# Performance work log

Hardware: AMD Instinct MI355X
Metric: run time of the kernel (lower is better)

The kernel has to match this reference:

```python
import jax, jax.numpy as jnp
import numpy as np

B, T, C = 2, 2048, 2048
N_HEAD, N_KV = 16, 4
HD = C // N_HEAD          # 128
ROPE_THETA = 10000.0


def setup_inputs() -> dict:
    key = jax.random.key(0)
    ks = jax.random.split(key, 6)
    std = 0.02
    x = jax.random.normal(ks[0], (B, T, C), dtype=jnp.float32)
    Wq = jax.random.normal(ks[1], (C, C), dtype=jnp.float32) * std
    Wk = jax.random.normal(ks[2], (C, N_KV * HD), dtype=jnp.float32) * std
    Wv = jax.random.normal(ks[3], (C, N_KV * HD), dtype=jnp.float32) * std
    Wo = jax.random.normal(ks[4], (C, C), dtype=jnp.float32) * std
    # real RoPE frequencies: freqs_cis = exp(i * t * theta^{-2j/hd})
    inv_freq = 1.0 / (ROPE_THETA ** (jnp.arange(0, HD, 2, dtype=jnp.float32) / HD))
    ang = jnp.arange(T, dtype=jnp.float32)[:, None] * inv_freq[None, :]  # [T, HD//2]
    return {"x": x, "Wq": Wq, "Wk": Wk, "Wv": Wv, "Wo": Wo,
            "freqs_cos": jnp.cos(ang), "freqs_sin": jnp.sin(ang)}


def _rope(t, cos, sin):
    # t: [B, H, T, HD]; cos/sin: [T, HD//2] -> complex rotate even/odd pairs
    tr = t.reshape(*t.shape[:-1], HD // 2, 2)
    re, im = tr[..., 0], tr[..., 1]
    c = cos[None, None, :, :]
    s = sin[None, None, :, :]
    out = jnp.stack([re * c - im * s, re * s + im * c], axis=-1)
    return out.reshape(t.shape)


def reference(x, Wq, Wk, Wv, Wo, freqs_cos, freqs_sin):
    Bm, Tm, Cm = x.shape
    q = (x @ Wq).reshape(Bm, Tm, N_HEAD, HD).transpose(0, 2, 1, 3)  # [B,H,T,HD]
    k = (x @ Wk).reshape(Bm, Tm, N_KV, HD).transpose(0, 2, 1, 3)    # [B,Hkv,T,HD]
    v = (x @ Wv).reshape(Bm, Tm, N_KV, HD).transpose(0, 2, 1, 3)
    q = _rope(q, freqs_cos, freqs_sin)
    k = _rope(k, freqs_cos, freqs_sin)
    rep = N_HEAD // N_KV
    k = jnp.repeat(k, rep, axis=1)  # GQA repeat_kv -> [B,H,T,HD]
    v = jnp.repeat(v, rep, axis=1)
    scale = 1.0 / jnp.sqrt(jnp.asarray(HD, dtype=x.dtype))
    att = jnp.einsum("bhqd,bhkd->bhqk", q, k) * scale
    causal = jnp.tril(jnp.ones((Tm, Tm), dtype=bool))
    att = jnp.where(causal[None, None], att, jnp.asarray(-jnp.inf, att.dtype))
    att = jax.nn.softmax(att, axis=-1)
    y = jnp.einsum("bhqk,bhkd->bhqd", att, v)
    y = y.transpose(0, 2, 1, 3).reshape(Bm, Tm, Cm)
    return y @ Wo
```

## Files before the change

### kernel.cpp

```cpp
#include <hip/hip_runtime.h>

#define B_ 2
#define T_ 2048
#define C_ 2048
#define NH_ 16
#define NKV_ 4
#define HD_ 128
#define REP_ (NH_ / NKV_)
#define LDQKV 3072

typedef unsigned short u16;
typedef __bf16 bf16x8v __attribute__((ext_vector_type(8)));
typedef float f32x4v __attribute__((ext_vector_type(4)));

__device__ __forceinline__ u16 f2bf(float f) {
    unsigned int u;
    __builtin_memcpy(&u, &f, 4);
    u += 0x7FFFu + ((u >> 16) & 1u);
    return (u16)(u >> 16);
}
__device__ __forceinline__ unsigned int pk2(float a, float b) {
    unsigned int ua, ub;
    __builtin_memcpy(&ua, &a, 4);
    __builtin_memcpy(&ub, &b, 4);
    ua += 0x8000u; ub += 0x8000u;
    return (ua >> 16) | (ub & 0xFFFF0000u);
}
__device__ __forceinline__ bf16x8v load8(const u16* p) {
    return *reinterpret_cast<const bf16x8v*>(p);
}
__device__ __forceinline__ void gl16(const u16* g, u16* l) {
    __builtin_amdgcn_global_load_lds(
        (const __attribute__((address_space(1))) void*)(g),
        (__attribute__((address_space(3))) void*)(l), 16, 0, 0);
}
__device__ __forceinline__ void stg(const u16* g, u16* l, int tid, int K) {
    gl16(g, l + tid * 8);
    gl16(g + (size_t)64 * K, l + 4096 + tid * 8);
}
__device__ __forceinline__ void stgB3(const u16* g, u16* l, int tid, int K) {
    gl16(g, l + tid * 8);
    gl16(g + (size_t)64 * K, l + 4096 + tid * 8);
    gl16(g + (size_t)128 * K, l + 8192 + tid * 8);
}
#define BAR()      __builtin_amdgcn_s_barrier()
#define LGKM0()    asm volatile("s_waitcnt lgkmcnt(0)" ::: "memory")
#define SCHED0()   __builtin_amdgcn_sched_barrier(0)
#define PRIO(x)    __builtin_amdgcn_s_setprio(x)

__global__ void cvt_f32_bf16(const float* __restrict__ in, u16* __restrict__ out, int n4) {
    int i = blockIdx.x * blockDim.x + threadIdx.x;
    if (i >= n4) return;
    float4 v = reinterpret_cast<const float4*>(in)[i];
    ushort4 o;
    o.x = f2bf(v.x); o.y = f2bf(v.y); o.z = f2bf(v.z); o.w = f2bf(v.w);
    reinterpret_cast<ushort4*>(out)[i] = o;
}

__global__ void xpose_f32_bf16(const float* __restrict__ in, u16* __restrict__ out,
                               int R, int Cc) {
    __shared__ u16 tile[32][33];
    int bx = blockIdx.x * 32, by = blockIdx.y * 32;
    int tx = threadIdx.x, ty = threadIdx.y;
    for (int i = 0; i < 32; i += 8)
        tile[ty + i][tx] = f2bf(in[(size_t)(by + ty + i) * Cc + bx + tx]);
    __syncthreads();
    for (int i = 0; i < 32; i += 8)
        out[(size_t)(bx + ty + i) * R + by + tx] = tile[tx][ty + i];
}

__global__ __launch_bounds__(512, 2) void gemm_qkv(const u16* __restrict__ A,
                                                   const u16* __restrict__ BT,
                                                   u16* __restrict__ Cq,
                                                   u16* __restrict__ vtb,
                                                   const float* __restrict__ cb,
                                                   const float* __restrict__ sb,
                                                   int M, int N, int K) {
    __shared__ __align__(16) u16 As[2][2][8192];
    __shared__ __align__(16) u16 Bs[2][12288];
    int tid = threadIdx.x;
    int lane = tid & 63, wave = tid >> 6;
    int wm = wave >> 2, wn = wave & 3;
    int m15 = lane & 15, quad = lane >> 4;

    int nbx = N / 192;
    int bid = blockIdx.x, cpx = gridDim.x >> 3;
    int swz = (bid & 7) * cpx + (bid >> 3);
    int m0 = (swz / nbx) * 256, n0 = (swz % nbx) * 192;

    int r_ = tid >> 3, c_ = tid & 7;
    const u16* gA0 = A + (size_t)(m0 + r_) * K + ((c_ ^ (r_ & 7)) * 8);
    const u16* gB0 = BT + (size_t)(n0 + r_) * K + ((c_ ^ (r_ & 7)) * 8);

    int sw8 = m15 & 7;
    int co0 = (quad ^ sw8) * 8;
    int co1 = ((4 + quad) ^ sw8) * 8;
    const u16* aB = &As[0][0][0] + wm * 8192 + m15 * 64;
    const u16* bB = &Bs[0][0] + (wn * 48 + m15) * 64;

    f32x4v acc[8][3] = {};
    int NT = K >> 6;

    stgB3(gB0, &Bs[0][0], tid, K);
    stg(gA0, &As[0][0][0], tid, K);
    stg(gA0 + (size_t)128 * K, &As[0][1][0], tid, K);
    stgB3(gB0 + 64, &Bs[1][0], tid, K);
    asm volatile("s_waitcnt vmcnt(3)" ::: "memory");
    SCHED0();
    BAR();

    for (int t = 0; t < NT; t++) {
        int d = t & 1;
        const u16* aT = aB + d * 16384;
        const u16* bT = bB + d * 12288;
        bf16x8v a0[4][2], a1[4][2], bv[3][2];

#pragma unroll
        for (int mt = 0; mt < 4; mt++) {
            a0[mt][0] = load8(aT + mt * 1024 + co0);
            a0[mt][1] = load8(aT + mt * 1024 + co1);
        }
#pragma unroll
        for (int nt = 0; nt < 2; nt++) {
            bv[nt][0] = load8(bT + nt * 1024 + co0);
            bv[nt][1] = load8(bT + nt * 1024 + co1);
        }
        if (t + 1 < NT) stg(gA0 + (t + 1) * 64, &As[1 - d][0][0], tid, K);
        BAR(); LGKM0(); SCHED0(); PRIO(1);
#pragma unroll
        for (int kc = 0; kc < 2; kc++)
#pragma unroll
            for (int mt = 0; mt < 4; mt++)
#pragma unroll
                for (int nt = 0; nt < 2; nt++)
                    acc[mt][nt] = __builtin_amdgcn_mfma_f32_16x16x32_bf16(
                        a0[mt][kc], bv[nt][kc], acc[mt][nt], 0, 0, 0);
        PRIO(0); BAR();

#pragma unroll
        for (int mt = 0; mt < 4; mt++) {
            a1[mt][0] = load8(aT + (mt + 4) * 1024 + co0);
            a1[mt][1] = load8(aT + (mt + 4) * 1024 + co1);
        }
        bv[2][0] = load8(bT + 2048 + co0);
        bv[2][1] = load8(bT + 2048 + co1);
        if (t + 1 < NT) stg(gA0 + (size_t)128 * K + (t + 1) * 64, &As[1 - d][1][0], tid, K);
        BAR(); LGKM0(); SCHED0(); PRIO(1);
#pragma unroll
        for (int kc = 0; kc < 2; kc++)
#pragma unroll
            for (int mt = 0; mt < 4; mt++)
#pragma unroll
                for (int nt = 0; nt < 2; nt++)
                    acc[mt + 4][nt] = __builtin_amdgcn_mfma_f32_16x16x32_bf16(
                        a1[mt][kc], bv[nt][kc], acc[mt + 4][nt], 0, 0, 0);
        PRIO(0); BAR();

        if (t + 2 < NT) stgB3(gB0 + (t + 2) * 64, &Bs[d][0], tid, K);
        PRIO(1);
#pragma unroll
        for (int kc = 0; kc < 2; kc++)
#pragma unroll
            for (int mt = 0; mt < 4; mt++)
                acc[mt][2] = __builtin_amdgcn_mfma_f32_16x16x32_bf16(
                    a0[mt][kc], bv[2][kc], acc[mt][2], 0, 0, 0);
#pragma unroll
        for (int kc = 0; kc < 2; kc++)
#pragma unroll
            for (int mt = 0; mt < 4; mt++)
                acc[mt + 4][2] = __builtin_amdgcn_mfma_f32_16x16x32_bf16(
                    a1[mt][kc], bv[2][kc], acc[mt + 4][2], 0, 0, 0);
        PRIO(0);
        if (t + 2 < NT) { asm volatile("s_waitcnt vmcnt(3)" ::: "memory"); }
        else            { asm volatile("s_waitcnt vmcnt(0)" ::: "memory"); }
        SCHED0();
        BAR();
    }

#pragma unroll
    for (int mt = 0; mt < 8; mt++)
#pragma unroll
        for (int nt = 0; nt < 3; nt++) {
            int c = n0 + wn * 48 + nt * 16 + m15;
            if (c >= 2560) {
                int hd = c - 2560;
                int mbase = m0 + wm * 128 + mt * 16 + quad * 4;
                int bb = mbase >> 11, tok = mbase & 2047;
                int g = (tok & 31) >> 2;
                int off = (tok & ~31) + ((g & 3) * 8 + (g >> 2) * 4);
                ushort4 pk;
                pk.x = f2bf(acc[mt][nt][0]);
                pk.y = f2bf(acc[mt][nt][1]);
                pk.z = f2bf(acc[mt][nt][2]);
                pk.w = f2bf(acc[mt][nt][3]);
                *reinterpret_cast<ushort4*>(vtb + ((size_t)bb * 512 + hd) * T_ + off) = pk;
            } else {
                int i = (c & 127) >> 1;
                float sgn = (c & 1) ? 1.f : -1.f;
#pragma unroll
                for (int r = 0; r < 4; r++) {
                    int mrow = m0 + wm * 128 + mt * 16 + quad * 4 + r;
                    int tok = mrow & 2047;
                    float cv = cb[tok * 64 + i];
                    float sv = sb[tok * 64 + i];
                    float v = acc[mt][nt][r];
                    float pval = __shfl_xor(v, 1, 64);
                    float outv = fmaf(v, cv, pval * sv * sgn);
                    Cq[(size_t)mrow * N + c] = f2bf(outv);
                }
            }
        }
}

__global__ __launch_bounds__(512, 2) void gemm_out(const u16* __restrict__ A,
                                                   const u16* __restrict__ BT,
                                                   float* __restrict__ C,
                                                   int M, int N, int K) {
    __shared__ __align__(16) u16 As2[2][8192];
    __shared__ __align__(16) u16 Bs2[2][2][8192];
    int tid = threadIdx.x;
    int lane = tid & 63, wave = tid >> 6;
    int wm = wave >> 2, wn = wave & 3;
    int m15 = lane & 15, quad = lane >> 4;

    int nbx = N >> 8;
    int bid = blockIdx.x, cpx = gridDim.x >> 3;
    int swz = (bid & 7) * cpx + (bid >> 3);
    int m0 = (swz / nbx) * 128, n0 = (swz % nbx) * 256;

    const u16* gA0 = A + (size_t)(m0 + (tid >> 3)) * K + (((tid & 7) ^ ((tid >> 3) & 7)) * 8);
    const u16* gB0 = BT + (size_t)(n0 + (tid >> 3)) * K + (((tid & 7) ^ ((tid >> 3) & 7)) * 8);

    int sw8 = m15 & 7;
    int co0 = (quad ^ sw8) * 8;
    int co1 = ((4 + quad) ^ sw8) * 8;
    const u16* aB = &As2[0][0] + (wm * 64 + m15) * 64;
    const u16* bB = &Bs2[0][0][0] + (wn >> 1) * 8192 + ((wn & 1) * 64 + m15) * 64;

    f32x4v acc[4][4] = {};
    int NT = K >> 6;

    stg(gB0, &Bs2[0][0][0], tid, K);
    stg(gB0 + (size_t)128 * K, &Bs2[0][1][0], tid, K);
    stg(gA0, &As2[0][0], tid, K);
    stg(gB0 + 64, &Bs2[1][0][0], tid, K);
    stg(gB0 + (size_t)128 * K + 64, &Bs2[1][1][0], tid, K);
    asm volatile("s_waitcnt vmcnt(4)" ::: "memory");
    SCHED0();
    BAR();

    for (int t = 0; t < NT; t++) {
        int d = t & 1;
        const u16* aT = aB + d * 8192;
        const u16* bT = bB + d * 16384;
        bf16x8v a0[2][2], a1[2][2], b0[2][2], b1[2][2];

#pragma unroll
        for (int mt = 0; mt < 2; mt++) {
            a0[mt][0] = load8(aT + mt * 1024 + co0);
            a0[mt][1] = load8(aT + mt * 1024 + co1);
        }
#pragma unroll
        for (int nt = 0; nt < 2; nt++) {
            b0[nt][0] = load8(bT + nt * 1024 + co0);
            b0[nt][1] = load8(bT + nt * 1024 + co1);
        }
        if (t + 1 < NT) stg(gA0 + (t + 1) * 64, &As2[1 - d][0], tid, K);
        BAR(); LGKM0(); SCHED0(); PRIO(1);
#pragma unroll
        for (int kc = 0; kc < 2; kc++)
#pragma unroll
            for (int mt = 0; mt < 2; mt++)
#pragma unroll
                for (int nt = 0; nt < 2; nt++)
                    acc[mt][nt] = __builtin_amdgcn_mfma_f32_16x16x32_bf16(
                        a0[mt][kc], b0[nt][kc], acc[mt][nt], 0, 0, 0);
        PRIO(0); BAR();

#pragma unroll
        for (int nt = 0; nt < 2; nt++) {
            b1[nt][0] = load8(bT + (nt + 2) * 1024 + co0);
            b1[nt][1] = load8(bT + (nt + 2) * 1024 + co1);
        }
        BAR(); LGKM0(); SCHED0(); PRIO(1);
#pragma unroll
        for (int kc = 0; kc < 2; kc++)
#pragma unroll
            for (int mt = 0; mt < 2; mt++)
#pragma unroll
                for (int nt = 0; nt < 2; nt++)
                    acc[mt][nt + 2] = __builtin_amdgcn_mfma_f32_16x16x32_bf16(
                        a0[mt][kc], b1[nt][kc], acc[mt][nt + 2], 0, 0, 0);
        PRIO(0); BAR();

#pragma unroll
        for (int mt = 0; mt < 2; mt++) {
            a1[mt][0] = load8(aT + (mt + 2) * 1024 + co0);
            a1[mt][1] = load8(aT + (mt + 2) * 1024 + co1);
        }
        if (t + 2 < NT) stg(gB0 + (t + 2) * 64, &Bs2[d][0][0], tid, K);
        BAR(); LGKM0(); SCHED0(); PRIO(1);
#pragma unroll
        for (int kc = 0; kc < 2; kc++)
#pragma unroll
            for (int mt = 0; mt < 2; mt++)
#pragma unroll
                for (int nt = 0; nt < 2; nt++)
                    acc[mt + 2][nt] = __builtin_amdgcn_mfma_f32_16x16x32_bf16(
                        a1[mt][kc], b0[nt][kc], acc[mt + 2][nt], 0, 0, 0);
        PRIO(0); BAR();

        if (t + 2 < NT) stg(gB0 + (size_t)128 * K + (t + 2) * 64, &Bs2[d][1][0], tid, K);
        BAR(); PRIO(1);
#pragma unroll
        for (int kc = 0; kc < 2; kc++)
#pragma unroll
            for (int mt = 0; mt < 2; mt++)
#pragma unroll
                for (int nt = 0; nt < 2; nt++)
                    acc[mt + 2][nt + 2] = __builtin_amdgcn_mfma_f32_16x16x32_bf16(
                        a1[mt][kc], b1[nt][kc], acc[mt + 2][nt + 2], 0, 0, 0);
        PRIO(0);
        if (t + 2 < NT) { asm volatile("s_waitcnt vmcnt(4)" ::: "memory"); }
        else            { asm volatile("s_waitcnt vmcnt(0)" ::: "memory"); }
        SCHED0();
        BAR();
    }

#pragma unroll
    for (int mt = 0; mt < 4; mt++)
#pragma unroll
        for (int nt = 0; nt < 4; nt++) {
            int c = n0 + wn * 64 + nt * 16 + m15;
#pragma unroll
            for (int r = 0; r < 4; r++) {
                int mrow = m0 + wm * 64 + mt * 16 + quad * 4 + r;
                C[(size_t)mrow * N + c] = acc[mt][nt][r];
            }
        }
}

__device__ __forceinline__ void stgK64(const u16* kB, u16* Kl, int kt, int tid) {
    int keyc = tid >> 4, ch = tid & 15;
    const u16* g = kB + (size_t)(kt + keyc) * LDQKV + (ch ^ keyc) * 8;
    u16* l = Kl + tid * 8;
#pragma unroll
    for (int j = 0; j < 4; j++) {
        gl16(g, l);
        g += (size_t)16 * LDQKV;
        l += 2048;
    }
}
__device__ __forceinline__ void stgV64(const u16* vB, u16* Vl, int kt, int tid) {
    int hdc = tid >> 3, ch = tid & 7;
    const u16* g = vB + (size_t)hdc * T_ + kt + (ch ^ (hdc & 7)) * 8;
    u16* l = Vl + tid * 8;
#pragma unroll
    for (int j = 0; j < 4; j++) {
        gl16(g, l);
        g += (size_t)32 * T_;
        l += 2048;
    }
}

__global__ __launch_bounds__(256) void flash_k(const u16* __restrict__ qkv,
                                               const u16* __restrict__ vtb,
                                               u16* __restrict__ yb) {
    __shared__ __align__(16) u16 Kl[2][64 * 128];
    __shared__ __align__(16) u16 Vl[2][128 * 64];
    int h = blockIdx.y, b = blockIdx.z;
    int kv = h / REP_;
    int tid = threadIdx.x;
    int lane = tid & 63, wave = tid >> 6;
    int m15 = lane & 15, quad = lane >> 4;
    int sw8 = m15 & 7;
    const u16* kB = qkv + (size_t)b * T_ * LDQKV + 2048 + kv * HD_;
    const u16* vB = vtb + ((size_t)(b * NKV_ + kv)) * HD_ * T_;
    const float scale2 = 0.1275173723f;
    const float M0b = 8.0f;
    const float NEG = -3.0e38f;

    for (int p = 0; p < 2; p++) {
        int qt = (p == 0) ? (int)blockIdx.x : (31 - (int)blockIdx.x);
        int qt0 = qt * 64;
        int q_i = qt0 + wave * 16 + m15;
        const u16* qp = qkv + (size_t)(b * T_ + q_i) * LDQKV + h * HD_ + quad * 8;
        bf16x8v qf[4];
#pragma unroll
        for (int kc = 0; kc < 4; kc++) qf[kc] = load8(qp + kc * 32);
        f32x4v o[8] = {};
        f32x4v lacc = {};
        int NT = qt + 1;

        stgK64(kB, &Kl[0][0], 0, tid);
        stgV64(vB, &Vl[0][0], 0, tid);
        stgK64(kB, &Kl[1][0], 64, tid);
        stgV64(vB, &Vl[1][0], 64, tid);
        asm volatile("s_waitcnt vmcnt(8)" ::: "memory");
        SCHED0();
        BAR();

        for (int it = 0; it < NT; it++) {
            int cur = it & 1;
            int kt = it * 64;
            const u16* Kc = &Kl[cur][0];
            const u16* Vc = &Vl[cur][0];

            bf16x8v kf[4][4];
#pragma unroll
            for (int nt = 0; nt < 4; nt++) {
                const u16* kls = Kc + (nt * 16 + m15) * 128;
#pragma unroll
                for (int kc = 0; kc < 4; kc++)
                    kf[nt][kc] = load8(kls + (((kc * 4 + quad) ^ m15) * 8));
            }
            if (it >= 1 && it + 1 < NT) stgK64(kB, &Kl[1 - cur][0], kt + 64, tid);
            BAR(); LGKM0(); SCHED0(); PRIO(1);
            f32x4v s4[4] = {};
#pragma unroll
            for (int nt = 0; nt < 4; nt++)
#pragma unroll
                for (int kc = 0; kc < 4; kc++)
                    s4[nt] = __builtin_amdgcn_mfma_f32_16x16x32_bf16(
                        kf[nt][kc], qf[kc], s4[nt], 0, 0, 0);
            PRIO(0);
            if (it + 1 < NT) { asm volatile("s_waitcnt vmcnt(4)" ::: "memory"); }
            else             { asm volatile("s_waitcnt vmcnt(0)" ::: "memory"); }
            SCHED0(); BAR();

            if (kt + 64 > qt0) {
#pragma unroll
                for (int nt = 0; nt < 4; nt++) {
                    int key = kt + nt * 16 + quad * 4;
#pragma unroll
                    for (int r = 0; r < 4; r++)
                        if (key + r > q_i) s4[nt][r] = NEG;
                }
            }
#pragma unroll
            for (int nt = 0; nt < 4; nt++) {
#pragma unroll
                for (int r = 0; r < 4; r++)
                    s4[nt][r] = exp2f(fmaf(s4[nt][r], scale2, -M0b));
                lacc += s4[nt];
            }
            bf16x8v pf[2];
#pragma unroll
            for (int c = 0; c < 2; c++) {
                unsigned int w[4];
                w[0] = pk2(s4[2 * c][0], s4[2 * c][1]);
                w[1] = pk2(s4[2 * c][2], s4[2 * c][3]);
                w[2] = pk2(s4[2 * c + 1][0], s4[2 * c + 1][1]);
                w[3] = pk2(s4[2 * c + 1][2], s4[2 * c + 1][3]);
                __builtin_memcpy(&pf[c], w, 16);
            }
            bf16x8v vf[2][8];
#pragma unroll
            for (int c = 0; c < 2; c++)
#pragma unroll
                for (int dt = 0; dt < 8; dt++)
                    vf[c][dt] = load8(Vc + (dt * 16 + m15) * 64 + (((c * 4 + quad) ^ sw8) * 8));
            if (it >= 1 && it + 1 < NT) stgV64(vB, &Vl[1 - cur][0], kt + 64, tid);
            BAR(); LGKM0(); SCHED0(); PRIO(1);
#pragma unroll
            for (int c = 0; c < 2; c++)
#pragma unroll
                for (int dt = 0; dt < 8; dt++)
                    o[dt] = __builtin_amdgcn_mfma_f32_16x16x32_bf16(
                        vf[c][dt], pf[c], o[dt], 0, 0, 0);
            PRIO(0);
            if (it + 1 < NT) { asm volatile("s_waitcnt vmcnt(4)" ::: "memory"); }
            SCHED0(); BAR();
        }

        float l = lacc[0] + lacc[1] + lacc[2] + lacc[3];
        l += __shfl_xor(l, 16, 64);
        l += __shfl_xor(l, 32, 64);
        float inv = 1.f / l;
        u16* yp = yb + (size_t)(b * T_ + q_i) * C_ + h * HD_ + quad * 4;
#pragma unroll
        for (int dt = 0; dt < 8; dt++) {
            ushort4 pk;
            pk.x = f2bf(o[dt][0] * inv);
            pk.y = f2bf(o[dt][1] * inv);
            pk.z = f2bf(o[dt][2] * inv);
            pk.w = f2bf(o[dt][3] * inv);
            *reinterpret_cast<ushort4*>(yp + dt * 16) = pk;
        }
    }
}

extern "C" void kernel_launch(void* const* d_in, const int* in_sizes, int n_in,
                              void* d_out, int out_size, void* d_ws, size_t ws_size,
                              hipStream_t stream) {
    const float* x  = (const float*)d_in[0];
    const float* Wq = (const float*)d_in[1];
    const float* Wk = (const float*)d_in[2];
    const float* Wv = (const float*)d_in[3];
    const float* Wo = (const float*)d_in[4];
    const float* fc = (const float*)d_in[5];
    const float* fs = (const float*)d_in[6];
    float* out = (float*)d_out;

    char* ws = (char*)d_ws;
    u16* WqkvT = (u16*)(ws);
    u16* WoT   = (u16*)(ws + 12582912);
    u16* xb    = (u16*)(ws + 20971520);
    u16* qkvb  = (u16*)(ws + 37748736);
    u16* vtb   = (u16*)(ws + 62914560);
    u16* yb    = (u16*)(ws + 67108864);

    const int M = B_ * T_;

    int n4 = (M * C_) / 4;
    cvt_f32_bf16<<<n4 / 256, 256, 0, stream>>>(x, xb, n4);

    dim3 tb(32, 8);
    xpose_f32_bf16<<<dim3(C_ / 32, C_ / 32), tb, 0, stream>>>(Wq, WqkvT, C_, C_);
    xpose_f32_bf16<<<dim3((NKV_ * HD_) / 32, C_ / 32), tb, 0, stream>>>(Wk, WqkvT + 2048 * 2048, C_, NKV_ * HD_);
    xpose_f32_bf16<<<dim3((NKV_ * HD_) / 32, C_ / 32), tb, 0, stream>>>(Wv, WqkvT + 2560 * 2048, C_, NKV_ * HD_);
    xpose_f32_bf16<<<dim3(C_ / 32, C_ / 32), tb, 0, stream>>>(Wo, WoT, C_, C_);

    gemm_qkv<<<dim3((LDQKV / 192) * (M / 256)), 512, 0, stream>>>(xb, WqkvT, qkvb, vtb, fc, fs, M, LDQKV, C_);

    flash_k<<<dim3(T_ / 128, NH_, B_), 256, 0, stream>>>(qkvb, vtb, yb);

    gemm_out<<<dim3((C_ / 256) * (M / 128)), 512, 0, stream>>>(yb, WoT, out, M, C_, C_);
}
```

Measured before the change: 289.7 us.

## Restructure attention KV double-buffer to one barrier per tile and use hardware bf16 pack

The attention loop now issues K and V prefetches for the next tile together at the start of each iteration. It waits on them once at the end, which cuts the per-iteration barriers from four to one and moves the V LDS reads up next to the QK MFMAs. The prologue now stages only the first tile and waits for it fully. The software round-and-pack bf16 conversion of probabilities is replaced by the v_cvt_pk_bf16_f32 instruction. Prefetch depth drops from two tiles ahead to one, and waiting with vmcnt(0) may expose global load latency on short causal rows.

```diff
diff --git a/kernel.cpp b/kernel.cpp
--- a/kernel.cpp
+++ b/kernel.cpp
@@ -19,12 +19,10 @@
     u += 0x7FFFu + ((u >> 16) & 1u);
     return (u16)(u >> 16);
 }
-__device__ __forceinline__ unsigned int pk2(float a, float b) {
-    unsigned int ua, ub;
-    __builtin_memcpy(&ua, &a, 4);
-    __builtin_memcpy(&ub, &b, 4);
-    ua += 0x8000u; ub += 0x8000u;
-    return (ua >> 16) | (ub & 0xFFFF0000u);
+__device__ __forceinline__ unsigned int cvtpk(float a, float b) {
+    unsigned int r;
+    asm("v_cvt_pk_bf16_f32 %0, %1, %2" : "=v"(r) : "v"(a), "v"(b));
+    return r;
 }
 __device__ __forceinline__ bf16x8v load8(const u16* p) {
     return *reinterpret_cast<const bf16x8v*>(p);
@@ -394,9 +392,7 @@
 
         stgK64(kB, &Kl[0][0], 0, tid);
         stgV64(vB, &Vl[0][0], 0, tid);
-        stgK64(kB, &Kl[1][0], 64, tid);
-        stgV64(vB, &Vl[1][0], 64, tid);
-        asm volatile("s_waitcnt vmcnt(8)" ::: "memory");
+        asm volatile("s_waitcnt vmcnt(0)" ::: "memory");
         SCHED0();
         BAR();
 
@@ -414,9 +410,13 @@
                 for (int kc = 0; kc < 4; kc++)
                     kf[nt][kc] = load8(kls + (((kc * 4 + quad) ^ m15) * 8));
             }
-            if (it >= 1 && it + 1 < NT) stgK64(kB, &Kl[1 - cur][0], kt + 64, tid);
-            BAR(); LGKM0(); SCHED0(); PRIO(1);
+            if (it + 1 < NT) {
+                stgK64(kB, &Kl[1 - cur][0], kt + 64, tid);
+                stgV64(vB, &Vl[1 - cur][0], kt + 64, tid);
+            }
+            SCHED0();
             f32x4v s4[4] = {};
+            PRIO(1);
 #pragma unroll
             for (int nt = 0; nt < 4; nt++)
 #pragma unroll
@@ -424,10 +424,12 @@
                     s4[nt] = __builtin_amdgcn_mfma_f32_16x16x32_bf16(
                         kf[nt][kc], qf[kc], s4[nt], 0, 0, 0);
             PRIO(0);
-            if (it + 1 < NT) { asm volatile("s_waitcnt vmcnt(4)" ::: "memory"); }
-            else             { asm volatile("s_waitcnt vmcnt(0)" ::: "memory"); }
-            SCHED0(); BAR();
-
+            bf16x8v vf[2][8];
+#pragma unroll
+            for (int c = 0; c < 2; c++)
+#pragma unroll
+                for (int dt = 0; dt < 8; dt++)
+                    vf[c][dt] = load8(Vc + (dt * 16 + m15) * 64 + (((c * 4 + quad) ^ sw8) * 8));
             if (kt + 64 > qt0) {
 #pragma unroll
                 for (int nt = 0; nt < 4; nt++) {
@@ -448,20 +450,13 @@
 #pragma unroll
             for (int c = 0; c < 2; c++) {
                 unsigned int w[4];
-                w[0] = pk2(s4[2 * c][0], s4[2 * c][1]);
-                w[1] = pk2(s4[2 * c][2], s4[2 * c][3]);
-                w[2] = pk2(s4[2 * c + 1][0], s4[2 * c + 1][1]);
-                w[3] = pk2(s4[2 * c + 1][2], s4[2 * c + 1][3]);
+                w[0] = cvtpk(s4[2 * c][0], s4[2 * c][1]);
+                w[1] = cvtpk(s4[2 * c][2], s4[2 * c][3]);
+                w[2] = cvtpk(s4[2 * c + 1][0], s4[2 * c + 1][1]);
+                w[3] = cvtpk(s4[2 * c + 1][2], s4[2 * c + 1][3]);
                 __builtin_memcpy(&pf[c], w, 16);
             }
-            bf16x8v vf[2][8];
-#pragma unroll
-            for (int c = 0; c < 2; c++)
-#pragma unroll
-                for (int dt = 0; dt < 8; dt++)
-                    vf[c][dt] = load8(Vc + (dt * 16 + m15) * 64 + (((c * 4 + quad) ^ sw8) * 8));
-            if (it >= 1 && it + 1 < NT) stgV64(vB, &Vl[1 - cur][0], kt + 64, tid);
-            BAR(); LGKM0(); SCHED0(); PRIO(1);
+            PRIO(1);
 #pragma unroll
             for (int c = 0; c < 2; c++)
 #pragma unroll
@@ -469,8 +464,9 @@
                     o[dt] = __builtin_amdgcn_mfma_f32_16x16x32_bf16(
                         vf[c][dt], pf[c], o[dt], 0, 0, 0);
             PRIO(0);
-            if (it + 1 < NT) { asm volatile("s_waitcnt vmcnt(4)" ::: "memory"); }
-            SCHED0(); BAR();
+            if (it + 1 < NT) { asm volatile("s_waitcnt vmcnt(0)" ::: "memory"); }
+            SCHED0();
+            BAR();
         }
 
         float l = lacc[0] + lacc[1] + lacc[2] + lacc[3];
```

Result: no change. 288.6 us (-0.4%).
